# Performance work log

Hardware: AMD Instinct MI355X
Metric: run time of the kernel (lower is better)

The kernel has to match this reference:

```python
import jax, jax.numpy as jnp
import numpy as np

N = 100000
E = 800000
D_IN = 256
D_H = 512


def setup_inputs() -> dict:
    key = jax.random.key(0)
    ks = jax.random.split(key, 8)
    s_in = 1.0 / np.sqrt(D_IN)
    s_h = 1.0 / np.sqrt(D_H)
    return {
        "x": jax.random.normal(ks[0], (N, D_IN), jnp.float32),
        "edge_index": jax.random.randint(ks[1], (2, E), 0, N, dtype=jnp.int64),
        "W1": jax.random.normal(ks[2], (D_IN, D_H), jnp.float32) * s_in,
        "b1": jnp.zeros((D_H,), jnp.float32),
        "W2": jax.random.normal(ks[3], (D_H, D_H), jnp.float32) * s_h,
        "b2": jnp.zeros((D_H,), jnp.float32),
        "W3": jax.random.normal(ks[4], (D_H, D_H), jnp.float32) * s_h,
        "b3": jnp.zeros((D_H,), jnp.float32),
        "Wfc": jax.random.normal(ks[5], (D_H, D_IN), jnp.float32) * s_h,
        "bfc": jnp.zeros((D_IN,), jnp.float32),
    }


def _gcn_prep(edge_index, n_nodes):
    # PyG GCNConv: add self-loops, symmetric deg^{-1/2} normalization.
    loop = jnp.arange(n_nodes, dtype=edge_index.dtype)
    row = jnp.concatenate([edge_index[0], loop])  # destination
    col = jnp.concatenate([edge_index[1], loop])  # source
    deg = jax.ops.segment_sum(jnp.ones_like(row, dtype=jnp.float32), row,
                              num_segments=n_nodes)
    dinv = jax.lax.rsqrt(deg)  # deg >= 1 due to self loops
    norm = dinv[row] * dinv[col]  # [E+N]
    return row, col, norm


def _gcn_conv(x, W, b, row, col, norm, n_nodes):
    h = x @ W  # [N, out]
    msg = h[col] * norm[:, None]  # [E+N, out] gather + scale
    out = jax.ops.segment_sum(msg, row, num_segments=n_nodes)  # scatter-add
    return out + b


def reference(x, edge_index, W1, b1, W2, b2, W3, b3, Wfc, bfc):
    n = x.shape[0]
    row, col, norm = _gcn_prep(edge_index, n)
    h = jax.nn.relu(_gcn_conv(x, W1, b1, row, col, norm, n))
    h = jax.nn.relu(_gcn_conv(h, W2, b2, row, col, norm, n))
    h = jax.nn.relu(_gcn_conv(h, W3, b3, row, col, norm, n))
    return h @ Wfc + bfc
```

## Files before the change

### kernel.cpp

```cpp
#include <hip/hip_runtime.h>

#define N_NODES 100000
#define NPAD    100096
#define E_EDGES 800000

typedef _Float16 f16;
typedef _Float16 f16x4 __attribute__((ext_vector_type(4)));
typedef _Float16 f16x8 __attribute__((ext_vector_type(8)));
typedef float    f32x4 __attribute__((ext_vector_type(4)));

__device__ inline void async16(const void* g, void* l) {
    __builtin_amdgcn_global_load_lds(
        (const __attribute__((address_space(1))) void*)g,
        (__attribute__((address_space(3))) void*)l, 16, 0, 0);
}

__global__ void k_deg(const int* __restrict__ ei, int* __restrict__ deg) {
    int e = blockIdx.x * 256 + threadIdx.x;
    if (e < E_EDGES) atomicAdd(&deg[ei[e]], 1);
}

__global__ void k_scan1(const int* __restrict__ deg, int* __restrict__ off,
                        int* __restrict__ bsum, float* __restrict__ dinv) {
    __shared__ int s[256];
    int i = blockIdx.x * 256 + threadIdx.x;
    int d = (i < N_NODES) ? deg[i] : 0;
    int pd = (d + 3) & ~3;
    dinv[i] = (i < N_NODES) ? rsqrtf((float)(d + 1)) : 0.f;
    s[threadIdx.x] = pd;
    __syncthreads();
    for (int dd = 1; dd < 256; dd <<= 1) {
        int t = (threadIdx.x >= dd) ? s[threadIdx.x - dd] : 0;
        __syncthreads();
        s[threadIdx.x] += t;
        __syncthreads();
    }
    if (i < N_NODES) off[i] = s[threadIdx.x] - pd;
    if (threadIdx.x == 255) bsum[blockIdx.x] = s[255];
}

__global__ void k_scan2(int* __restrict__ bsum, int nb) {
    __shared__ int s[512];
    int tid = threadIdx.x;
    int v = (tid < nb) ? bsum[tid] : 0;
    s[tid] = v;
    __syncthreads();
    for (int d = 1; d < 512; d <<= 1) {
        int t = (tid >= d) ? s[tid - d] : 0;
        __syncthreads();
        s[tid] += t;
        __syncthreads();
    }
    if (tid < nb) bsum[tid] = s[tid] - v;
}

__global__ void k_scan3(int* __restrict__ off, const int* __restrict__ bsum,
                        const int* __restrict__ deg, int* __restrict__ csr) {
    int i = blockIdx.x * 256 + threadIdx.x;
    if (i >= N_NODES) return;
    int o = off[i] + bsum[blockIdx.x];
    off[i] = o;
    int d = deg[i], pd = (d + 3) & ~3;
    for (int k = d; k < pd; ++k) csr[o + k] = NPAD;
    if (i == N_NODES - 1) off[N_NODES] = o + pd;
}

__global__ void k_fill(const int* __restrict__ ei, const int* __restrict__ off,
                       int* __restrict__ cursor, int* __restrict__ csr) {
    int e = blockIdx.x * 256 + threadIdx.x;
    if (e >= E_EDGES) return;
    int dst = ei[e];
    int src = ei[E_EDGES + e];
    int pos = atomicAdd(&cursor[dst], 1);
    csr[off[dst] + pos] = src;
}

__global__ void k_x_to_f16(const float* __restrict__ x,
                           const float* __restrict__ dinv,
                           f16* __restrict__ xh) {
    int i = blockIdx.x * 256 + threadIdx.x;
    if (i >= N_NODES * 64) return;
    float d = dinv[i >> 6];
    float4 v = ((const float4*)x)[i];
    f16x4 o;
    o.x = (f16)(v.x * d); o.y = (f16)(v.y * d);
    o.z = (f16)(v.z * d); o.w = (f16)(v.w * d);
    ((f16x4*)xh)[i] = o;
}

__global__ void k_transpose(const float* __restrict__ W, f16* __restrict__ Wt,
                            int K, int M) {
    int m = blockIdx.x * 256 + threadIdx.x;
    int k = blockIdx.y;
    if (m < M) Wt[(size_t)m * K + k] = (f16)W[(size_t)k * M + m];
}

template<int K, int M, int MODE>
__launch_bounds__(256, 2)
__global__ void k_gemm(const f16* __restrict__ A, const f16* __restrict__ B,
                       void* __restrict__ C, const float* __restrict__ bias,
                       const float* __restrict__ dsc) {
    __shared__ __align__(16) char smem[16384];
    f16* As = (f16*)smem;
    f16* Bs = (f16*)(smem + 8192);
    int tid  = threadIdx.x;
    int wave = tid >> 6, lane = tid & 63;
    int wr = (wave >> 1) * 64, wc = (wave & 1) * 64;
    int lm = lane & 15, q = lane >> 4;
    int rowBase = blockIdx.x * 128;
    int colBase = blockIdx.y * 128;

    f32x4 acc[4][4] = {};
    const f16* Ag = A + (size_t)rowBase * K;
    const f16* Bg = B + (size_t)colBase * K;

    int c0 = tid, c1 = tid + 256;
    for (int kt = 0; kt < K; kt += 32) {
        __syncthreads();
        async16(Ag + (size_t)(c0 >> 2) * K + kt + (c0 & 3) * 8, &As[c0 * 8]);
        async16(Ag + (size_t)(c1 >> 2) * K + kt + (c1 & 3) * 8, &As[c1 * 8]);
        async16(Bg + (size_t)(c0 >> 2) * K + kt + (c0 & 3) * 8, &Bs[c0 * 8]);
        async16(Bg + (size_t)(c1 >> 2) * K + kt + (c1 & 3) * 8, &Bs[c1 * 8]);
        __syncthreads();

        f16x8 a[4], b[4];
#pragma unroll
        for (int i = 0; i < 4; ++i) {
            a[i] = *(const f16x8*)&As[(wr + i * 16 + lm) * 32 + q * 8];
            b[i] = *(const f16x8*)&Bs[(wc + i * 16 + lm) * 32 + q * 8];
        }
#pragma unroll
        for (int i = 0; i < 4; ++i)
#pragma unroll
            for (int j = 0; j < 4; ++j)
                acc[i][j] = __builtin_amdgcn_mfma_f32_16x16x32_f16(
                    a[i], b[j], acc[i][j], 0, 0, 0);
    }

    if (MODE == 2) {
#pragma unroll
        for (int i = 0; i < 4; ++i) {
            int gr0 = rowBase + wr + i * 16 + q * 4;
#pragma unroll
            for (int j = 0; j < 4; ++j) {
                int gc = colBase + wc + j * 16 + lm;
                float bj = bias[gc];
#pragma unroll
                for (int r = 0; r < 4; ++r) {
                    int gr = gr0 + r;
                    if (gr < N_NODES)
                        ((float*)C)[(size_t)gr * M + gc] = acc[i][j][r] + bj;
                }
            }
        }
    } else {
        __syncthreads();
        f16* Ep = (f16*)smem + wave * (16 * 80);
#pragma unroll
        for (int i = 0; i < 4; ++i) {
            f32x4 dr = {1.f, 1.f, 1.f, 1.f};
            if (MODE == 3)
                dr = *(const f32x4*)&dsc[rowBase + wr + i * 16 + q * 4];
#pragma unroll
            for (int j = 0; j < 4; ++j) {
                int colg = colBase + wc + j * 16 + lm;
#pragma unroll
                for (int r = 0; r < 4; ++r) {
                    float v = acc[i][j][r];
                    if (MODE == 1) {
                        v += bias[colg];
                        v = v > 0.f ? v : 0.f;
                    }
                    if (MODE == 3) v *= dr[r];
                    Ep[(q * 4 + r) * 80 + j * 16 + lm] = (f16)v;
                }
            }
            __syncthreads();
            int row0 = lane >> 3, c8 = lane & 7;
            f16x8 v0 = *(const f16x8*)&Ep[row0 * 80 + c8 * 8];
            f16x8 v1 = *(const f16x8*)&Ep[(row0 + 8) * 80 + c8 * 8];
            int gr0 = rowBase + wr + i * 16 + row0;
            int gc  = colBase + wc + c8 * 8;
            *(f16x8*)&((f16*)C)[(size_t)gr0 * M + gc] = v0;
            *(f16x8*)&((f16*)C)[(size_t)(gr0 + 8) * M + gc] = v1;
            __syncthreads();
        }
    }
}

template<int VE> struct VecT;
template<> struct VecT<4> { typedef f16x4 type; };
template<> struct VecT<8> { typedef f16x8 type; };

template<int CH, bool ACT>
__launch_bounds__(256)
__global__ void k_agg(const f16* __restrict__ t, const int* __restrict__ off,
                      const int* __restrict__ csr, const float* __restrict__ dinv,
                      const float* __restrict__ bias, f16* __restrict__ h) {
    constexpr int VE = CH / 64;
    typedef typename VecT<VE>::type vec;
    int node = blockIdx.x * 4 + (threadIdx.x >> 6);
    if (node >= N_NODES) return;
    int lane = threadIdx.x & 63;
    const vec* __restrict__ rows = (const vec*)t;

    vec v = rows[node * 64 + lane];
    float acc[VE];
#pragma unroll
    for (int j = 0; j < VE; ++j) acc[j] = (float)v[j];

    int s = off[node], e = off[node + 1];
    if (s < e) {
        int4 iv = *(const int4*)&csr[s];
        for (int idx = s; idx < e; idx += 4) {
            int4 nxt = *(const int4*)&csr[idx + 4];
            vec u0 = rows[iv.x * 64 + lane];
            vec u1 = rows[iv.y * 64 + lane];
            vec u2 = rows[iv.z * 64 + lane];
            vec u3 = rows[iv.w * 64 + lane];
            iv = nxt;
#pragma unroll
            for (int j = 0; j < VE; ++j)
                acc[j] += ((float)u0[j] + (float)u1[j])
                        + ((float)u2[j] + (float)u3[j]);
        }
    }

    float di = dinv[node];
    vec o;
#pragma unroll
    for (int j = 0; j < VE; ++j) {
        float r = di * acc[j];
        if (ACT) {
            r += bias[lane * VE + j];
            r = r > 0.f ? r : 0.f;
        }
        o[j] = (f16)r;
    }
    ((vec*)h)[node * 64 + lane] = o;
}

extern "C" void kernel_launch(void* const* d_in, const int* in_sizes, int n_in,
                              void* d_out, int out_size, void* d_ws, size_t ws_size,
                              hipStream_t stream) {
    const float* x   = (const float*)d_in[0];
    const int*   ei  = (const int*)d_in[1];
    const float* W1  = (const float*)d_in[2];
    const float* b1  = (const float*)d_in[3];
    const float* W2  = (const float*)d_in[4];
    const float* b2  = (const float*)d_in[5];
    const float* W3  = (const float*)d_in[6];
    const float* b3  = (const float*)d_in[7];
    const float* Wfc = (const float*)d_in[8];
    const float* bfc = (const float*)d_in[9];

    char* wsb = (char*)d_ws;
    size_t o = 0;
    auto alloc = [&](size_t bytes) -> void* {
        void* p = wsb + o;
        o += (bytes + 255) & ~(size_t)255;
        return p;
    };

    f16* xh   = (f16*)alloc((size_t)(NPAD + 1) * 256 * 2);
    f16* t    = (f16*)alloc((size_t)(NPAD + 1) * 512 * 2);
    f16* h    = (f16*)alloc((size_t)NPAD * 512 * 2);
    f16* Wt1  = (f16*)alloc(512 * 256 * 2);
    f16* Wt2  = (f16*)alloc(512 * 512 * 2);
    f16* Wt3  = (f16*)alloc(512 * 512 * 2);
    f16* Wtfc = (f16*)alloc(256 * 512 * 2);
    int* deg    = (int*)alloc(N_NODES * 4);
    float* dinv = (float*)alloc(NPAD * 4);
    int* off    = (int*)alloc((N_NODES + 1) * 4);
    int* cursor = (int*)alloc(N_NODES * 4);
    int* bsum   = (int*)alloc(4096 * 4);
    int* csr    = (int*)alloc(((size_t)E_EDGES + 3 * N_NODES + 8) * 4);

    f16* a1 = t;

    const int NB = (N_NODES + 255) / 256;

    hipMemsetAsync(deg, 0, N_NODES * 4, stream);
    hipMemsetAsync(cursor, 0, N_NODES * 4, stream);
    hipMemsetAsync(xh + (size_t)NPAD * 256, 0, 256 * 2, stream);
    hipMemsetAsync(t  + (size_t)NPAD * 512, 0, 512 * 2, stream);

    k_deg<<<(E_EDGES + 255) / 256, 256, 0, stream>>>(ei, deg);
    k_scan1<<<NB, 256, 0, stream>>>(deg, off, bsum, dinv);
    k_scan2<<<1, 512, 0, stream>>>(bsum, NB);
    k_scan3<<<NB, 256, 0, stream>>>(off, bsum, deg, csr);
    k_fill<<<(E_EDGES + 255) / 256, 256, 0, stream>>>(ei, off, cursor, csr);

    k_x_to_f16<<<(N_NODES * 64 + 255) / 256, 256, 0, stream>>>(x, dinv, xh);
    k_transpose<<<dim3(2, 256), 256, 0, stream>>>(W1, Wt1, 256, 512);
    k_transpose<<<dim3(2, 512), 256, 0, stream>>>(W2, Wt2, 512, 512);
    k_transpose<<<dim3(2, 512), 256, 0, stream>>>(W3, Wt3, 512, 512);
    k_transpose<<<dim3(1, 512), 256, 0, stream>>>(Wfc, Wtfc, 512, 256);

    dim3 g4(NPAD / 128, 4), g2(NPAD / 128, 2);
    const int AGG_GRID = N_NODES / 4;

    k_agg<256, false><<<AGG_GRID, 256, 0, stream>>>(xh, off, csr, dinv, nullptr, a1);
    k_gemm<256, 512, 1><<<g4, 256, 0, stream>>>(a1, Wt1, h, b1, nullptr);
    k_gemm<512, 512, 3><<<g4, 256, 0, stream>>>(h, Wt2, t, nullptr, dinv);
    k_agg<512, true><<<AGG_GRID, 256, 0, stream>>>(t, off, csr, dinv, b2, h);
    k_gemm<512, 512, 3><<<g4, 256, 0, stream>>>(h, Wt3, t, nullptr, dinv);
    k_agg<512, true><<<AGG_GRID, 256, 0, stream>>>(t, off, csr, dinv, b3, h);
    k_gemm<512, 256, 2><<<g2, 256, 0, stream>>>(h, Wtfc, d_out, bfc, nullptr);
}
```

Baseline: 918.6 us.

## Remap GEMM workgroups per XCD and unroll aggregation to eight neighbors

```diff
diff --git a/kernel.cpp b/kernel.cpp
--- a/kernel.cpp
+++ b/kernel.cpp
@@ -107,8 +107,16 @@
     int wave = tid >> 6, lane = tid & 63;
     int wr = (wave >> 1) * 64, wc = (wave & 1) * 64;
     int lm = lane & 15, q = lane >> 4;
-    int rowBase = blockIdx.x * 128;
-    int colBase = blockIdx.y * 128;
+
+    constexpr int CB  = M / 128;
+    constexpr int NWG = (NPAD / 128) * CB;
+    constexpr int Q   = NWG / 8, R = NWG % 8;
+    int id  = blockIdx.x;
+    int xcd = id & 7, pos = id >> 3;
+    int nid = (xcd < R) ? xcd * (Q + 1) + pos
+                        : R * (Q + 1) + (xcd - R) * Q + pos;
+    int rowBase = (nid / CB) * 128;
+    int colBase = (nid % CB) * 128;
 
     f32x4 acc[4][4] = {};
     const f16* Ag = A + (size_t)rowBase * K;
@@ -193,37 +201,51 @@
 template<> struct VecT<8> { typedef f16x8 type; };
 
 template<int CH, bool ACT>
-__launch_bounds__(256)
+__launch_bounds__(64)
 __global__ void k_agg(const f16* __restrict__ t, const int* __restrict__ off,
                       const int* __restrict__ csr, const float* __restrict__ dinv,
                       const float* __restrict__ bias, f16* __restrict__ h) {
     constexpr int VE = CH / 64;
     typedef typename VecT<VE>::type vec;
-    int node = blockIdx.x * 4 + (threadIdx.x >> 6);
-    if (node >= N_NODES) return;
-    int lane = threadIdx.x & 63;
+    int node = blockIdx.x;
+    int lane = threadIdx.x;
     const vec* __restrict__ rows = (const vec*)t;
 
-    vec v = rows[node * 64 + lane];
+    vec v = rows[(size_t)node * 64 + lane];
     float acc[VE];
 #pragma unroll
     for (int j = 0; j < VE; ++j) acc[j] = (float)v[j];
 
     int s = off[node], e = off[node + 1];
-    if (s < e) {
-        int4 iv = *(const int4*)&csr[s];
-        for (int idx = s; idx < e; idx += 4) {
-            int4 nxt = *(const int4*)&csr[idx + 4];
-            vec u0 = rows[iv.x * 64 + lane];
-            vec u1 = rows[iv.y * 64 + lane];
-            vec u2 = rows[iv.z * 64 + lane];
-            vec u3 = rows[iv.w * 64 + lane];
-            iv = nxt;
-#pragma unroll
-            for (int j = 0; j < VE; ++j)
-                acc[j] += ((float)u0[j] + (float)u1[j])
-                        + ((float)u2[j] + (float)u3[j]);
-        }
+    int idx = s;
+    for (; idx + 8 <= e; idx += 8) {
+        int4 ia = *(const int4*)&csr[idx];
+        int4 ib = *(const int4*)&csr[idx + 4];
+        vec u0 = rows[(size_t)ia.x * 64 + lane];
+        vec u1 = rows[(size_t)ia.y * 64 + lane];
+        vec u2 = rows[(size_t)ia.z * 64 + lane];
+        vec u3 = rows[(size_t)ia.w * 64 + lane];
+        vec u4 = rows[(size_t)ib.x * 64 + lane];
+        vec u5 = rows[(size_t)ib.y * 64 + lane];
+        vec u6 = rows[(size_t)ib.z * 64 + lane];
+        vec u7 = rows[(size_t)ib.w * 64 + lane];
+#pragma unroll
+        for (int j = 0; j < VE; ++j)
+            acc[j] += (((float)u0[j] + (float)u1[j])
+                     + ((float)u2[j] + (float)u3[j]))
+                    + (((float)u4[j] + (float)u5[j])
+                     + ((float)u6[j] + (float)u7[j]));
+    }
+    if (idx < e) {
+        int4 ia = *(const int4*)&csr[idx];
+        vec u0 = rows[(size_t)ia.x * 64 + lane];
+        vec u1 = rows[(size_t)ia.y * 64 + lane];
+        vec u2 = rows[(size_t)ia.z * 64 + lane];
+        vec u3 = rows[(size_t)ia.w * 64 + lane];
+#pragma unroll
+        for (int j = 0; j < VE; ++j)
+            acc[j] += ((float)u0[j] + (float)u1[j])
+                    + ((float)u2[j] + (float)u3[j]);
     }
 
     float di = dinv[node];
@@ -237,7 +259,7 @@
         }
         o[j] = (f16)r;
     }
-    ((vec*)h)[node * 64 + lane] = o;
+    ((vec*)h)[(size_t)node * 64 + lane] = o;
 }
 
 extern "C" void kernel_launch(void* const* d_in, const int* in_sizes, int n_in,
@@ -297,14 +319,14 @@
     k_transpose<<<dim3(2, 512), 256, 0, stream>>>(W3, Wt3, 512, 512);
     k_transpose<<<dim3(1, 512), 256, 0, stream>>>(Wfc, Wtfc, 512, 256);
 
-    dim3 g4(NPAD / 128, 4), g2(NPAD / 128, 2);
-    const int AGG_GRID = N_NODES / 4;
-
-    k_agg<256, false><<<AGG_GRID, 256, 0, stream>>>(xh, off, csr, dinv, nullptr, a1);
-    k_gemm<256, 512, 1><<<g4, 256, 0, stream>>>(a1, Wt1, h, b1, nullptr);
-    k_gemm<512, 512, 3><<<g4, 256, 0, stream>>>(h, Wt2, t, nullptr, dinv);
-    k_agg<512, true><<<AGG_GRID, 256, 0, stream>>>(t, off, csr, dinv, b2, h);
-    k_gemm<512, 512, 3><<<g4, 256, 0, stream>>>(h, Wt3, t, nullptr, dinv);
-    k_agg<512, true><<<AGG_GRID, 256, 0, stream>>>(t, off, csr, dinv, b3, h);
-    k_gemm<512, 256, 2><<<g2, 256, 0, stream>>>(h, Wtfc, d_out, bfc, nullptr);
-}
+    constexpr int NWG4 = (NPAD / 128) * 4;
+    constexpr int NWG2 = (NPAD / 128) * 2;
+
+    k_agg<256, false><<<N_NODES, 64, 0, stream>>>(xh, off, csr, dinv, nullptr, a1);
+    k_gemm<256, 512, 1><<<NWG4, 256, 0, stream>>>(a1, Wt1, h, b1, nullptr);
+    k_gemm<512, 512, 3><<<NWG4, 256, 0, stream>>>(h, Wt2, t, nullptr, dinv);
+    k_agg<512, true><<<N_NODES, 64, 0, stream>>>(t, off, csr, dinv, b2, h);
+    k_gemm<512, 512, 3><<<NWG4, 256, 0, stream>>>(h, Wt3, t, nullptr, dinv);
+    k_agg<512, true><<<N_NODES, 64, 0, stream>>>(t, off, csr, dinv, b3, h);
+    k_gemm<512, 256, 2><<<NWG2, 256, 0, stream>>>(h, Wtfc, d_out, bfc, nullptr);
+}
```

Measured after the change: 883.7 us. 1.04x faster.

## Remap GEMM workgroups per XCD, drop epilogue barriers, raise occupancy

Applied to the files above, without the earlier changes.

```diff
diff --git a/kernel.cpp b/kernel.cpp
--- a/kernel.cpp
+++ b/kernel.cpp
@@ -96,7 +96,7 @@
 }
 
 template<int K, int M, int MODE>
-__launch_bounds__(256, 2)
+__launch_bounds__(256, 3)
 __global__ void k_gemm(const f16* __restrict__ A, const f16* __restrict__ B,
                        void* __restrict__ C, const float* __restrict__ bias,
                        const float* __restrict__ dsc) {
@@ -107,8 +107,16 @@
     int wave = tid >> 6, lane = tid & 63;
     int wr = (wave >> 1) * 64, wc = (wave & 1) * 64;
     int lm = lane & 15, q = lane >> 4;
-    int rowBase = blockIdx.x * 128;
-    int colBase = blockIdx.y * 128;
+
+    constexpr int CB  = M / 128;
+    constexpr int NWG = (NPAD / 128) * CB;
+    constexpr int Q   = NWG / 8, R = NWG % 8;
+    int id  = blockIdx.x;
+    int xcd = id & 7, pos = id >> 3;
+    int nid = (xcd < R) ? xcd * (Q + 1) + pos
+                        : R * (Q + 1) + (xcd - R) * Q + pos;
+    int rowBase = (nid / CB) * 128;
+    int colBase = (nid % CB) * 128;
 
     f32x4 acc[4][4] = {};
     const f16* Ag = A + (size_t)rowBase * K;
@@ -175,7 +183,6 @@
                     Ep[(q * 4 + r) * 80 + j * 16 + lm] = (f16)v;
                 }
             }
-            __syncthreads();
             int row0 = lane >> 3, c8 = lane & 7;
             f16x8 v0 = *(const f16x8*)&Ep[row0 * 80 + c8 * 8];
             f16x8 v1 = *(const f16x8*)&Ep[(row0 + 8) * 80 + c8 * 8];
@@ -183,7 +190,6 @@
             int gc  = colBase + wc + c8 * 8;
             *(f16x8*)&((f16*)C)[(size_t)gr0 * M + gc] = v0;
             *(f16x8*)&((f16*)C)[(size_t)(gr0 + 8) * M + gc] = v1;
-            __syncthreads();
         }
     }
 }
@@ -204,7 +210,7 @@
     int lane = threadIdx.x & 63;
     const vec* __restrict__ rows = (const vec*)t;
 
-    vec v = rows[node * 64 + lane];
+    vec v = rows[(size_t)node * 64 + lane];
     float acc[VE];
 #pragma unroll
     for (int j = 0; j < VE; ++j) acc[j] = (float)v[j];
@@ -214,10 +220,10 @@
         int4 iv = *(const int4*)&csr[s];
         for (int idx = s; idx < e; idx += 4) {
             int4 nxt = *(const int4*)&csr[idx + 4];
-            vec u0 = rows[iv.x * 64 + lane];
-            vec u1 = rows[iv.y * 64 + lane];
-            vec u2 = rows[iv.z * 64 + lane];
-            vec u3 = rows[iv.w * 64 + lane];
+            vec u0 = rows[(size_t)iv.x * 64 + lane];
+            vec u1 = rows[(size_t)iv.y * 64 + lane];
+            vec u2 = rows[(size_t)iv.z * 64 + lane];
+            vec u3 = rows[(size_t)iv.w * 64 + lane];
             iv = nxt;
 #pragma unroll
             for (int j = 0; j < VE; ++j)
@@ -237,7 +243,7 @@
         }
         o[j] = (f16)r;
     }
-    ((vec*)h)[node * 64 + lane] = o;
+    ((vec*)h)[(size_t)node * 64 + lane] = o;
 }
 
 extern "C" void kernel_launch(void* const* d_in, const int* in_sizes, int n_in,
@@ -297,14 +303,15 @@
     k_transpose<<<dim3(2, 512), 256, 0, stream>>>(W3, Wt3, 512, 512);
     k_transpose<<<dim3(1, 512), 256, 0, stream>>>(Wfc, Wtfc, 512, 256);
 
-    dim3 g4(NPAD / 128, 4), g2(NPAD / 128, 2);
+    constexpr int NWG4 = (NPAD / 128) * 4;
+    constexpr int NWG2 = (NPAD / 128) * 2;
     const int AGG_GRID = N_NODES / 4;
 
     k_agg<256, false><<<AGG_GRID, 256, 0, stream>>>(xh, off, csr, dinv, nullptr, a1);
-    k_gemm<256, 512, 1><<<g4, 256, 0, stream>>>(a1, Wt1, h, b1, nullptr);
-    k_gemm<512, 512, 3><<<g4, 256, 0, stream>>>(h, Wt2, t, nullptr, dinv);
+    k_gemm<256, 512, 1><<<NWG4, 256, 0, stream>>>(a1, Wt1, h, b1, nullptr);
+    k_gemm<512, 512, 3><<<NWG4, 256, 0, stream>>>(h, Wt2, t, nullptr, dinv);
     k_agg<512, true><<<AGG_GRID, 256, 0, stream>>>(t, off, csr, dinv, b2, h);
-    k_gemm<512, 512, 3><<<g4, 256, 0, stream>>>(h, Wt3, t, nullptr, dinv);
+    k_gemm<512, 512, 3><<<NWG4, 256, 0, stream>>>(h, Wt3, t, nullptr, dinv);
     k_agg<512, true><<<AGG_GRID, 256, 0, stream>>>(t, off, csr, dinv, b3, h);
-    k_gemm<512, 256, 2><<<g2, 256, 0, stream>>>(h, Wtfc, d_out, bfc, nullptr);
-}
+    k_gemm<512, 256, 2><<<NWG2, 256, 0, stream>>>(h, Wtfc, d_out, bfc, nullptr);
+}
```

Result: faster. 894.7 us (-2.6%).
